# Kernel tuning notes

Measured on AMD Instinct MI355X. Metric: run time of the kernel, lower is better.

## Reference

```python
import jax, jax.numpy as jnp
import numpy as np

N = 50000
E = 625000
D = 128
L = 3
BN_EPS = 1e-5


def setup_inputs() -> dict:
    key = jax.random.key(0)
    ks = jax.random.split(key, 12)
    x = jax.random.normal(ks[0], (N, D), dtype=jnp.float32)
    edge_index = jax.random.randint(ks[1], (2, E), 0, N, dtype=jnp.int64)
    s = 1.0 / np.sqrt(D)
    W1 = jax.random.uniform(ks[2], (L, D, D), jnp.float32, -s, s)
    b1 = jax.random.uniform(ks[3], (L, D), jnp.float32, -s, s)
    W2 = jax.random.uniform(ks[4], (L, D, D), jnp.float32, -s, s)
    b2 = jax.random.uniform(ks[5], (L, D), jnp.float32, -s, s)
    eps = jnp.zeros((L,), jnp.float32)  # GINConv train_eps init 0
    gamma = jnp.ones((L, D), jnp.float32)
    beta = jnp.zeros((L, D), jnp.float32)
    Wl = jax.random.uniform(ks[6], (L, D, D), jnp.float32, -s, s)
    bl = jax.random.uniform(ks[7], (L, D), jnp.float32, -s, s)
    return {"x": x, "edge_index": edge_index, "W1": W1, "b1": b1, "W2": W2,
            "b2": b2, "eps": eps, "gamma": gamma, "beta": beta, "Wl": Wl, "bl": bl}


def reference(x, edge_index, W1, b1, W2, b2, eps, gamma, beta, Wl, bl):
    src, dst = edge_index[0], edge_index[1]
    xs = [x]
    h = x
    for i in range(L):
        # GIN aggregation: sum of neighbor (source) features at target nodes
        agg = jax.ops.segment_sum(h[src], dst, num_segments=N)  # [N, D]
        z = (1.0 + eps[i]) * h + agg
        # MLP: Linear -> ReLU -> Linear
        z = jax.nn.relu(z @ W1[i] + b1[i]) @ W2[i] + b2[i]
        # BatchNorm1d (training mode: batch stats, biased variance)
        mu = jnp.mean(z, axis=0)
        var = jnp.mean((z - mu) ** 2, axis=0)
        z = gamma[i] * (z - mu) * jax.lax.rsqrt(var + BN_EPS) + beta[i]
        if i != 0:
            z = z + xs[-1]
        h = jax.nn.relu(z)
        xs.append(h)
    outs = [xs[i + 1] @ Wl[i] + bl[i] for i in range(L)]
    return jnp.concatenate(outs, axis=-1)  # [N, L*D]
```

## Files before the change

### kernel.cpp

```cpp
#include <hip/hip_runtime.h>
#include <hip/hip_bf16.h>
#include <stdint.h>

#define NN 50000
#define NE 625000
#define DD 128
#define NL 3
#define GB 391

typedef __bf16 bf16x8 __attribute__((ext_vector_type(8)));
typedef float f32x4 __attribute__((ext_vector_type(4)));

__device__ __forceinline__ float bflo(uint32_t u) { return __uint_as_float(u << 16); }
__device__ __forceinline__ float bfhi(uint32_t u) { return __uint_as_float(u & 0xffff0000u); }
__device__ __forceinline__ uint16_t f2bf(float f) {
    __hip_bfloat16 h = __float2bfloat16(f);
    return __builtin_bit_cast(uint16_t, h);
}
__device__ __forceinline__ uint32_t pack2(float lo, float hi) {
    return (uint32_t)f2bf(lo) | ((uint32_t)f2bf(hi) << 16);
}

__global__ void k_hist(const int* __restrict__ dstv, int* __restrict__ deg) {
    int e = blockIdx.x * 256 + threadIdx.x;
    if (e < NE) atomicAdd(&deg[dstv[e]], 1);
}

__global__ __launch_bounds__(512) void k_scan1(int* __restrict__ cursor ,
                                               int* __restrict__ rowptr,
                                               int* __restrict__ rowend,
                                               int* __restrict__ gcount) {
    __shared__ int s[512];
    __shared__ int base;
    int t = threadIdx.x;
    int i = blockIdx.x * 512 + t;
    int v = (i < NN) ? cursor[i] : 0;
    s[t] = v;
    __syncthreads();
    for (int st = 1; st < 512; st <<= 1) {
        int a = (t >= st) ? s[t - st] : 0;
        __syncthreads();
        s[t] += a;
        __syncthreads();
    }
    if (t == 511) base = atomicAdd(gcount, s[511]);
    __syncthreads();
    if (i < NN) {
        int b = base + s[t] - v;
        rowptr[i] = b;
        rowend[i] = b + v;
        cursor[i] = b;
    }
}

__global__ void k_fill(const int* __restrict__ srcv, const int* __restrict__ dstv,
                       int* __restrict__ cursor, int* __restrict__ colv) {
    int e = blockIdx.x * 256 + threadIdx.x;
    if (e < NE) {
        int d = dstv[e];
        int p = atomicAdd(&cursor[d], 1);
        colv[p] = srcv[e];
    }
}

#define WCONV_BLOCKS 576
__global__ void k_prep(const float* __restrict__ x, uint16_t* __restrict__ hb,
                       int* __restrict__ cursor, int* __restrict__ gcount,
                       const float* __restrict__ W1, const float* __restrict__ W2,
                       const float* __restrict__ Wl, uint16_t* __restrict__ Wb) {
    int b = blockIdx.x;
    if (b < WCONV_BLOCKS) {
        int id = b * 256 + threadIdx.x;
        int m = id >> 14;
        int r = id & 16383;
        int k = r >> 7;
        int col = r & 127;
        const float* src;
        if (m < 3) src = W1 + m * 16384;
        else if (m < 6) src = W2 + (m - 3) * 16384;
        else src = Wl + (m - 6) * 16384;
        float v = src[k * 128 + col];
        Wb[m * 16384 + col * 128 + (k ^ ((col & 7) << 3))] = f2bf(v);
        return;
    }
    int id = (b - WCONV_BLOCKS) * 256 + threadIdx.x;
    if (id == 0) *gcount = 0;
    if (id < NN) cursor[id] = 0;
    int base = id * 4;
    if (base >= NN * DD) return;
    float4 v = *(const float4*)(x + base);
    uint2 st;
    st.x = pack2(v.x, v.y);
    st.y = pack2(v.z, v.w);
    *(uint2*)(hb + base) = st;
}

#define ACC8(u) \
    a0 += bflo(u.x); a1 += bfhi(u.x); a2 += bflo(u.y); a3 += bfhi(u.y); \
    a4 += bflo(u.z); a5 += bfhi(u.z); a6 += bflo(u.w); a7 += bfhi(u.w);

__global__ __launch_bounds__(256) void k_agg(const uint16_t* __restrict__ hb,
                                             const int* __restrict__ rowptr,
                                             const int* __restrict__ rowend,
                                             const int* __restrict__ colv,
                                             const float* __restrict__ epsp, int layer,
                                             uint16_t* __restrict__ zb,
                                             float* __restrict__ bnsum) {
    if (blockIdx.x == 0) bnsum[threadIdx.x] = 0.f;
    int g = (blockIdx.x * 256 + threadIdx.x) >> 4;
    int l16 = threadIdx.x & 15;
    if (g >= NN) return;
    float onepe = 1.0f + epsp[layer];
    int beg = rowptr[g], end = rowend[g];
    const uint4* hp = (const uint4*)hb;
    float a0 = 0.f, a1 = 0.f, a2 = 0.f, a3 = 0.f, a4 = 0.f, a5 = 0.f, a6 = 0.f, a7 = 0.f;
    int j = beg;
    for (; j + 7 < end; j += 8) {
        int s0 = colv[j];
        int s1 = colv[j + 1];
        int s2 = colv[j + 2];
        int s3 = colv[j + 3];
        int s4 = colv[j + 4];
        int s5 = colv[j + 5];
        int s6 = colv[j + 6];
        int s7 = colv[j + 7];
        uint4 u0 = hp[(size_t)s0 * 16 + l16];
        uint4 u1 = hp[(size_t)s1 * 16 + l16];
        uint4 u2 = hp[(size_t)s2 * 16 + l16];
        uint4 u3 = hp[(size_t)s3 * 16 + l16];
        uint4 u4 = hp[(size_t)s4 * 16 + l16];
        uint4 u5 = hp[(size_t)s5 * 16 + l16];
        uint4 u6 = hp[(size_t)s6 * 16 + l16];
        uint4 u7 = hp[(size_t)s7 * 16 + l16];
        ACC8(u0) ACC8(u1) ACC8(u2) ACC8(u3)
        ACC8(u4) ACC8(u5) ACC8(u6) ACC8(u7)
    }
    for (; j + 3 < end; j += 4) {
        int s0 = colv[j];
        int s1 = colv[j + 1];
        int s2 = colv[j + 2];
        int s3 = colv[j + 3];
        uint4 u0 = hp[(size_t)s0 * 16 + l16];
        uint4 u1 = hp[(size_t)s1 * 16 + l16];
        uint4 u2 = hp[(size_t)s2 * 16 + l16];
        uint4 u3 = hp[(size_t)s3 * 16 + l16];
        ACC8(u0) ACC8(u1) ACC8(u2) ACC8(u3)
    }
    for (; j < end; ++j) {
        int s0 = colv[j];
        uint4 u = hp[(size_t)s0 * 16 + l16];
        ACC8(u)
    }
    uint4 hu = hp[(size_t)g * 16 + l16];
    a0 = fmaf(onepe, bflo(hu.x), a0); a1 = fmaf(onepe, bfhi(hu.x), a1);
    a2 = fmaf(onepe, bflo(hu.y), a2); a3 = fmaf(onepe, bfhi(hu.y), a3);
    a4 = fmaf(onepe, bflo(hu.z), a4); a5 = fmaf(onepe, bfhi(hu.z), a5);
    a6 = fmaf(onepe, bflo(hu.w), a6); a7 = fmaf(onepe, bfhi(hu.w), a7);
    uint4 st;
    st.x = pack2(a0, a1); st.y = pack2(a2, a3);
    st.z = pack2(a4, a5); st.w = pack2(a6, a7);
    ((uint4*)zb)[(size_t)g * 16 + l16] = st;
}

__global__ __launch_bounds__(256) void k_mlp(const uint16_t* __restrict__ A,
                                             const uint16_t* __restrict__ W1img,
                                             const uint16_t* __restrict__ W2img,
                                             const float* __restrict__ b1,
                                             const float* __restrict__ b2,
                                             float* __restrict__ bnsum,
                                             uint16_t* __restrict__ z2b) {
    __shared__ uint16_t ldsW[16384];
    __shared__ uint16_t ldsT[16384];
    int tid = threadIdx.x;
    int wid = tid >> 6, lane = tid & 63;

    bf16x8 w2r[8];
#pragma unroll
    for (int it = 0; it < 8; ++it) w2r[it] = *(const bf16x8*)(W2img + (it * 256 + tid) * 8);

#pragma unroll
    for (int it = 0; it < 8; ++it) {
        int idx = (it * 256 + tid) * 8;
        *(bf16x8*)(&ldsW[idx]) = *(const bf16x8*)(W1img + idx);
    }
    __syncthreads();

    const int brow = blockIdx.x * 128;
    const int m0 = wid * 32;
    const int l15 = lane & 15;
    const int lhi = lane >> 4;

    f32x4 acc[2][8];
    f32x4 zero = {0.f, 0.f, 0.f, 0.f};
#pragma unroll
    for (int m = 0; m < 2; ++m)
#pragma unroll
        for (int n = 0; n < 8; ++n) acc[m][n] = zero;

    const char* Ab = (const char*)A;
#pragma unroll
    for (int kk = 0; kk < 4; ++kk) {
        int kbyte = kk * 64 + (lhi << 4);
        bf16x8 afrag[2];
#pragma unroll
        for (int m = 0; m < 2; ++m) {
            int row = brow + m0 + m * 16 + l15;
            if (row >= NN) row = NN - 1;
            afrag[m] = *(const bf16x8*)(Ab + (size_t)row * 256 + kbyte);
        }
#pragma unroll
        for (int n = 0; n < 8; ++n) {
            int col = n * 16 + l15;
            int addr = col * 256 + (kbyte ^ ((col & 7) << 4));
            bf16x8 bfrag = *(const bf16x8*)((const char*)ldsW + addr);
            acc[0][n] = __builtin_amdgcn_mfma_f32_16x16x32_bf16(afrag[0], bfrag, acc[0][n], 0, 0, 0);
            acc[1][n] = __builtin_amdgcn_mfma_f32_16x16x32_bf16(afrag[1], bfrag, acc[1][n], 0, 0, 0);
        }
    }

    {
        float bc[8];
#pragma unroll
        for (int n = 0; n < 8; ++n) bc[n] = b1[n * 16 + l15];
#pragma unroll
        for (int m = 0; m < 2; ++m) {
            int rbase = m0 + m * 16 + (lhi << 2);
#pragma unroll
            for (int r = 0; r < 4; ++r) {
                int row = rbase + r;
#pragma unroll
                for (int n = 0; n < 8; ++n) {
                    float v = fmaxf(acc[m][n][r] + bc[n], 0.f);
                    int col = n * 16 + l15;
                    int byteoff = row * 256 + ((col * 2) ^ ((row & 7) << 4));
                    *(uint16_t*)((char*)ldsT + byteoff) = f2bf(v);
                }
            }
        }
    }
    __syncthreads();

#pragma unroll
    for (int it = 0; it < 8; ++it) *(bf16x8*)(&ldsW[(it * 256 + tid) * 8]) = w2r[it];
    __syncthreads();

#pragma unroll
    for (int m = 0; m < 2; ++m)
#pragma unroll
        for (int n = 0; n < 8; ++n) acc[m][n] = zero;

#pragma unroll
    for (int kk = 0; kk < 4; ++kk) {
        int kbyte = kk * 64 + (lhi << 4);
        bf16x8 afrag[2];
#pragma unroll
        for (int m = 0; m < 2; ++m) {
            int rowl = m0 + m * 16 + l15;
            afrag[m] = *(const bf16x8*)((const char*)ldsT + rowl * 256 + (kbyte ^ ((rowl & 7) << 4)));
        }
#pragma unroll
        for (int n = 0; n < 8; ++n) {
            int col = n * 16 + l15;
            int addr = col * 256 + (kbyte ^ ((col & 7) << 4));
            bf16x8 bfrag = *(const bf16x8*)((const char*)ldsW + addr);
            acc[0][n] = __builtin_amdgcn_mfma_f32_16x16x32_bf16(afrag[0], bfrag, acc[0][n], 0, 0, 0);
            acc[1][n] = __builtin_amdgcn_mfma_f32_16x16x32_bf16(afrag[1], bfrag, acc[1][n], 0, 0, 0);
        }
    }

    float bc2[8];
#pragma unroll
    for (int n = 0; n < 8; ++n) bc2[n] = b2[n * 16 + l15];

    float s1[8], s2[8];
#pragma unroll
    for (int n = 0; n < 8; ++n) { s1[n] = 0.f; s2[n] = 0.f; }

#pragma unroll
    for (int m = 0; m < 2; ++m) {
        int rbase = brow + m0 + m * 16 + (lhi << 2);
#pragma unroll
        for (int r = 0; r < 4; ++r) {
            int row = rbase + r;
            bool ok = row < NN;
#pragma unroll
            for (int n = 0; n < 8; ++n) {
                float v = acc[m][n][r] + bc2[n];
                if (ok) {
                    z2b[(size_t)row * 128 + n * 16 + l15] = f2bf(v);
                    s1[n] += v;
                    s2[n] += v * v;
                }
            }
        }
    }

    __syncthreads();
    float* ls = (float*)ldsT;
    ls[tid] = 0.f;
    __syncthreads();
#pragma unroll
    for (int n = 0; n < 8; ++n) {
        float a1 = s1[n] + __shfl_xor(s1[n], 16);
        a1 += __shfl_xor(a1, 32);
        float a2 = s2[n] + __shfl_xor(s2[n], 16);
        a2 += __shfl_xor(a2, 32);
        if (lane < 16) {
            atomicAdd(&ls[n * 16 + lane], a1);
            atomicAdd(&ls[128 + n * 16 + lane], a2);
        }
    }
    __syncthreads();
    atomicAdd(&bnsum[tid], ls[tid]);
}

__global__ __launch_bounds__(256) void k_apply(const uint16_t* __restrict__ z2b,
                                               const uint16_t* __restrict__ hin,
                                               const float* __restrict__ bnsum,
                                               const float* __restrict__ gamma,
                                               const float* __restrict__ beta, int layer,
                                               uint16_t* __restrict__ hout) {
    __shared__ float sA[128], sB[128];
    int tid = threadIdx.x;
    if (tid < 128) {
        float mu = bnsum[tid] * (1.0f / NN);
        float var = bnsum[128 + tid] * (1.0f / NN) - mu * mu;
        float a = gamma[layer * 128 + tid] * rsqrtf(var + 1e-5f);
        sA[tid] = a;
        sB[tid] = beta[layer * 128 + tid] - mu * a;
    }
    __syncthreads();
    int id = blockIdx.x * 256 + tid;
    int base = id * 4;
    if (base >= NN * DD) return;
    int c = base & 127;
    uint2 zu = *(const uint2*)(z2b + base);
    float4 av = *(const float4*)(sA + c);
    float4 bv = *(const float4*)(sB + c);
    float v0 = fmaf(av.x, bflo(zu.x), bv.x);
    float v1 = fmaf(av.y, bfhi(zu.x), bv.y);
    float v2 = fmaf(av.z, bflo(zu.y), bv.z);
    float v3 = fmaf(av.w, bfhi(zu.y), bv.w);
    if (layer > 0) {
        uint2 h = *(const uint2*)(hin + base);
        v0 += bflo(h.x);
        v1 += bfhi(h.x);
        v2 += bflo(h.y);
        v3 += bfhi(h.y);
    }
    v0 = fmaxf(v0, 0.f);
    v1 = fmaxf(v1, 0.f);
    v2 = fmaxf(v2, 0.f);
    v3 = fmaxf(v3, 0.f);
    uint2 st;
    st.x = pack2(v0, v1);
    st.y = pack2(v2, v3);
    *(uint2*)(hout + base) = st;
}

__global__ __launch_bounds__(256) void k_outgemm(const uint16_t* __restrict__ h1,
                                                 const uint16_t* __restrict__ h2,
                                                 const uint16_t* __restrict__ h3,
                                                 const uint16_t* __restrict__ Wb6,
                                                 const float* __restrict__ bl,
                                                 float* __restrict__ out) {
    __shared__ uint16_t lds[16384];
    int layer = blockIdx.x / GB;
    int blk = blockIdx.x - layer * GB;
    const uint16_t* A = (layer == 0) ? h1 : ((layer == 1) ? h2 : h3);
    const uint16_t* Wimg = Wb6 + layer * 16384;
    const float* bias = bl + layer * 128;

    int tid = threadIdx.x;
    int wid = tid >> 6, lane = tid & 63;
#pragma unroll
    for (int it = 0; it < 8; ++it) {
        int idx = (it * 256 + tid) * 8;
        bf16x8 v = *(const bf16x8*)(Wimg + idx);
        *(bf16x8*)(&lds[idx]) = v;
    }
    __syncthreads();

    const int brow = blk * 128;
    const int m0 = wid * 32;
    const int l15 = lane & 15;
    const int lhi = lane >> 4;

    f32x4 acc[2][8];
    f32x4 zero = {0.f, 0.f, 0.f, 0.f};
#pragma unroll
    for (int m = 0; m < 2; ++m)
#pragma unroll
        for (int n = 0; n < 8; ++n) acc[m][n] = zero;

    const char* Ab = (const char*)A;
#pragma unroll
    for (int kk = 0; kk < 4; ++kk) {
        int kbyte = kk * 64 + (lhi << 4);
        bf16x8 afrag[2];
#pragma unroll
        for (int m = 0; m < 2; ++m) {
            int row = brow + m0 + m * 16 + l15;
            if (row >= NN) row = NN - 1;
            afrag[m] = *(const bf16x8*)(Ab + (size_t)row * 256 + kbyte);
        }
#pragma unroll
        for (int n = 0; n < 8; ++n) {
            int col = n * 16 + l15;
            int addr = col * 256 + (kbyte ^ ((col & 7) << 4));
            bf16x8 bfrag = *(const bf16x8*)((const char*)lds + addr);
            acc[0][n] = __builtin_amdgcn_mfma_f32_16x16x32_bf16(afrag[0], bfrag, acc[0][n], 0, 0, 0);
            acc[1][n] = __builtin_amdgcn_mfma_f32_16x16x32_bf16(afrag[1], bfrag, acc[1][n], 0, 0, 0);
        }
    }

    float bcol[8];
#pragma unroll
    for (int n = 0; n < 8; ++n) bcol[n] = bias[n * 16 + l15];

#pragma unroll
    for (int m = 0; m < 2; ++m) {
        int rbase = brow + m0 + m * 16 + (lhi << 2);
#pragma unroll
        for (int r = 0; r < 4; ++r) {
            int row = rbase + r;
            if (row < NN) {
#pragma unroll
                for (int n = 0; n < 8; ++n) {
                    float v = acc[m][n][r] + bcol[n];
                    out[(size_t)row * (NL * DD) + layer * 128 + n * 16 + l15] = v;
                }
            }
        }
    }
}

extern "C" void kernel_launch(void* const* d_in, const int* in_sizes, int n_in,
                              void* d_out, int out_size, void* d_ws, size_t ws_size,
                              hipStream_t stream) {
    const float* x = (const float*)d_in[0];
    const int* ei = (const int*)d_in[1];
    const float* W1 = (const float*)d_in[2];
    const float* b1 = (const float*)d_in[3];
    const float* W2 = (const float*)d_in[4];
    const float* b2 = (const float*)d_in[5];
    const float* epsp = (const float*)d_in[6];
    const float* gamma = (const float*)d_in[7];
    const float* beta = (const float*)d_in[8];
    const float* Wl = (const float*)d_in[9];
    const float* bl = (const float*)d_in[10];
    float* out = (float*)d_out;

    char* w = (char*)d_ws;
    size_t off = 0;
    auto take = [&](size_t b) -> char* {
        char* p = w + off;
        off += (b + 255) & ~(size_t)255;
        return p;
    };
    uint16_t* hb[4];
    for (int i = 0; i < 4; ++i) hb[i] = (uint16_t*)take((size_t)NN * DD * 2);
    uint16_t* zb = (uint16_t*)take((size_t)NN * DD * 2);
    uint16_t* z2b = (uint16_t*)take((size_t)NN * DD * 2);
    int* rowptr = (int*)take((size_t)NN * 4);
    int* rowend = (int*)take((size_t)NN * 4);
    int* cursor = (int*)take((size_t)NN * 4);
    int* colv = (int*)take((size_t)NE * 4);
    uint16_t* Wb = (uint16_t*)take(9 * 16384 * 2);
    float* bnsum = (float*)take(256 * 4);
    int* gcount = (int*)take(256);

    const int* srcv = ei;
    const int* dstv = ei + NE;

    const int x2bf_blocks = (NN * DD / 4 + 255) / 256;
    k_prep<<<WCONV_BLOCKS + x2bf_blocks, 256, 0, stream>>>(x, hb[0], cursor, gcount,
                                                           W1, W2, Wl, Wb);

    k_hist<<<(NE + 255) / 256, 256, 0, stream>>>(dstv, cursor);
    k_scan1<<<98, 512, 0, stream>>>(cursor, rowptr, rowend, gcount);
    k_fill<<<(NE + 255) / 256, 256, 0, stream>>>(srcv, dstv, cursor, colv);

    const int agg_blocks = (NN * 16 + 255) / 256;

    for (int l = 0; l < NL; ++l) {
        k_agg<<<agg_blocks, 256, 0, stream>>>(hb[l], rowptr, rowend, colv, epsp, l, zb, bnsum);
        k_mlp<<<GB, 256, 0, stream>>>(zb, Wb + l * 16384, Wb + (3 + l) * 16384,
                                      b1 + l * 128, b2 + l * 128, bnsum, z2b);
        k_apply<<<x2bf_blocks, 256, 0, stream>>>(z2b, hb[l], bnsum, gamma, beta,
                                                 l, hb[l + 1]);
    }
    k_outgemm<<<NL * GB, 256, 0, stream>>>(hb[1], hb[2], hb[3], Wb + 6 * 16384, bl, out);
}
```

Before: 266.2 us.

## Fuse aggregation into MLP kernel and BN-apply into output GEMM

```diff
diff --git a/kernel.cpp b/kernel.cpp
--- a/kernel.cpp
+++ b/kernel.cpp
@@ -66,6 +66,7 @@
 #define WCONV_BLOCKS 576
 __global__ void k_prep(const float* __restrict__ x, uint16_t* __restrict__ hb,
                        int* __restrict__ cursor, int* __restrict__ gcount,
+                       float* __restrict__ bnsum,
                        const float* __restrict__ W1, const float* __restrict__ W2,
                        const float* __restrict__ Wl, uint16_t* __restrict__ Wb) {
     int b = blockIdx.x;
@@ -85,6 +86,7 @@
     }
     int id = (b - WCONV_BLOCKS) * 256 + threadIdx.x;
     if (id == 0) *gcount = 0;
+    if (id < NL * 256) bnsum[id] = 0.f;
     if (id < NN) cursor[id] = 0;
     int base = id * 4;
     if (base >= NN * DD) return;
@@ -95,97 +97,110 @@
     *(uint2*)(hb + base) = st;
 }
 
-#define ACC8(u) \
-    a0 += bflo(u.x); a1 += bfhi(u.x); a2 += bflo(u.y); a3 += bfhi(u.y); \
-    a4 += bflo(u.z); a5 += bfhi(u.z); a6 += bflo(u.w); a7 += bfhi(u.w);
-
-__global__ __launch_bounds__(256) void k_agg(const uint16_t* __restrict__ hb,
-                                             const int* __restrict__ rowptr,
-                                             const int* __restrict__ rowend,
-                                             const int* __restrict__ colv,
-                                             const float* __restrict__ epsp, int layer,
-                                             uint16_t* __restrict__ zb,
-                                             float* __restrict__ bnsum) {
-    if (blockIdx.x == 0) bnsum[threadIdx.x] = 0.f;
-    int g = (blockIdx.x * 256 + threadIdx.x) >> 4;
-    int l16 = threadIdx.x & 15;
-    if (g >= NN) return;
-    float onepe = 1.0f + epsp[layer];
-    int beg = rowptr[g], end = rowend[g];
-    const uint4* hp = (const uint4*)hb;
-    float a0 = 0.f, a1 = 0.f, a2 = 0.f, a3 = 0.f, a4 = 0.f, a5 = 0.f, a6 = 0.f, a7 = 0.f;
-    int j = beg;
-    for (; j + 7 < end; j += 8) {
-        int s0 = colv[j];
-        int s1 = colv[j + 1];
-        int s2 = colv[j + 2];
-        int s3 = colv[j + 3];
-        int s4 = colv[j + 4];
-        int s5 = colv[j + 5];
-        int s6 = colv[j + 6];
-        int s7 = colv[j + 7];
-        uint4 u0 = hp[(size_t)s0 * 16 + l16];
-        uint4 u1 = hp[(size_t)s1 * 16 + l16];
-        uint4 u2 = hp[(size_t)s2 * 16 + l16];
-        uint4 u3 = hp[(size_t)s3 * 16 + l16];
-        uint4 u4 = hp[(size_t)s4 * 16 + l16];
-        uint4 u5 = hp[(size_t)s5 * 16 + l16];
-        uint4 u6 = hp[(size_t)s6 * 16 + l16];
-        uint4 u7 = hp[(size_t)s7 * 16 + l16];
-        ACC8(u0) ACC8(u1) ACC8(u2) ACC8(u3)
-        ACC8(u4) ACC8(u5) ACC8(u6) ACC8(u7)
-    }
-    for (; j + 3 < end; j += 4) {
-        int s0 = colv[j];
-        int s1 = colv[j + 1];
-        int s2 = colv[j + 2];
-        int s3 = colv[j + 3];
-        uint4 u0 = hp[(size_t)s0 * 16 + l16];
-        uint4 u1 = hp[(size_t)s1 * 16 + l16];
-        uint4 u2 = hp[(size_t)s2 * 16 + l16];
-        uint4 u3 = hp[(size_t)s3 * 16 + l16];
-        ACC8(u0) ACC8(u1) ACC8(u2) ACC8(u3)
-    }
-    for (; j < end; ++j) {
-        int s0 = colv[j];
-        uint4 u = hp[(size_t)s0 * 16 + l16];
-        ACC8(u)
-    }
-    uint4 hu = hp[(size_t)g * 16 + l16];
-    a0 = fmaf(onepe, bflo(hu.x), a0); a1 = fmaf(onepe, bfhi(hu.x), a1);
-    a2 = fmaf(onepe, bflo(hu.y), a2); a3 = fmaf(onepe, bfhi(hu.y), a3);
-    a4 = fmaf(onepe, bflo(hu.z), a4); a5 = fmaf(onepe, bfhi(hu.z), a5);
-    a6 = fmaf(onepe, bflo(hu.w), a6); a7 = fmaf(onepe, bfhi(hu.w), a7);
-    uint4 st;
-    st.x = pack2(a0, a1); st.y = pack2(a2, a3);
-    st.z = pack2(a4, a5); st.w = pack2(a6, a7);
-    ((uint4*)zb)[(size_t)g * 16 + l16] = st;
-}
-
-__global__ __launch_bounds__(256) void k_mlp(const uint16_t* __restrict__ A,
-                                             const uint16_t* __restrict__ W1img,
-                                             const uint16_t* __restrict__ W2img,
-                                             const float* __restrict__ b1,
-                                             const float* __restrict__ b2,
-                                             float* __restrict__ bnsum,
-                                             uint16_t* __restrict__ z2b) {
+__global__ __launch_bounds__(256) void k_aggmlp(const uint16_t* __restrict__ hb,
+                                                const int* __restrict__ rowptr,
+                                                const int* __restrict__ rowend,
+                                                const int* __restrict__ colv,
+                                                const float* __restrict__ epsp, int layer,
+                                                const uint16_t* __restrict__ W1img,
+                                                const uint16_t* __restrict__ W2img,
+                                                const float* __restrict__ b1,
+                                                const float* __restrict__ b2,
+                                                float* __restrict__ bnsum,
+                                                uint16_t* __restrict__ z2b) {
     __shared__ uint16_t ldsW[16384];
     __shared__ uint16_t ldsT[16384];
     int tid = threadIdx.x;
     int wid = tid >> 6, lane = tid & 63;
-
-    bf16x8 w2r[8];
-#pragma unroll
-    for (int it = 0; it < 8; ++it) w2r[it] = *(const bf16x8*)(W2img + (it * 256 + tid) * 8);
+    const int brow = blockIdx.x * 128;
 
 #pragma unroll
     for (int it = 0; it < 8; ++it) {
         int idx = (it * 256 + tid) * 8;
         *(bf16x8*)(&ldsW[idx]) = *(const bf16x8*)(W1img + idx);
     }
-    __syncthreads();
-
-    const int brow = blockIdx.x * 128;
+
+    int row = tid >> 1, half = tid & 1;
+    int g = brow + row;
+    float a[64];
+#pragma unroll
+    for (int i = 0; i < 64; ++i) a[i] = 0.f;
+    if (g < NN) {
+        float onepe = 1.0f + epsp[layer];
+        int beg = rowptr[g], end = rowend[g];
+        const uint4* hp = (const uint4*)hb + half * 8;
+        int j = beg;
+        for (; j + 1 < end; j += 2) {
+            int s0 = colv[j];
+            int s1 = colv[j + 1];
+            const uint4* r0 = hp + (size_t)s0 * 16;
+            const uint4* r1 = hp + (size_t)s1 * 16;
+            uint4 u[8], v[8];
+#pragma unroll
+            for (int i = 0; i < 8; ++i) u[i] = r0[i];
+#pragma unroll
+            for (int i = 0; i < 8; ++i) v[i] = r1[i];
+#pragma unroll
+            for (int i = 0; i < 8; ++i) {
+                a[i * 8 + 0] += bflo(u[i].x); a[i * 8 + 1] += bfhi(u[i].x);
+                a[i * 8 + 2] += bflo(u[i].y); a[i * 8 + 3] += bfhi(u[i].y);
+                a[i * 8 + 4] += bflo(u[i].z); a[i * 8 + 5] += bfhi(u[i].z);
+                a[i * 8 + 6] += bflo(u[i].w); a[i * 8 + 7] += bfhi(u[i].w);
+            }
+#pragma unroll
+            for (int i = 0; i < 8; ++i) {
+                a[i * 8 + 0] += bflo(v[i].x); a[i * 8 + 1] += bfhi(v[i].x);
+                a[i * 8 + 2] += bflo(v[i].y); a[i * 8 + 3] += bfhi(v[i].y);
+                a[i * 8 + 4] += bflo(v[i].z); a[i * 8 + 5] += bfhi(v[i].z);
+                a[i * 8 + 6] += bflo(v[i].w); a[i * 8 + 7] += bfhi(v[i].w);
+            }
+        }
+        if (j < end) {
+            int s0 = colv[j];
+            const uint4* r0 = hp + (size_t)s0 * 16;
+            uint4 u[8];
+#pragma unroll
+            for (int i = 0; i < 8; ++i) u[i] = r0[i];
+#pragma unroll
+            for (int i = 0; i < 8; ++i) {
+                a[i * 8 + 0] += bflo(u[i].x); a[i * 8 + 1] += bfhi(u[i].x);
+                a[i * 8 + 2] += bflo(u[i].y); a[i * 8 + 3] += bfhi(u[i].y);
+                a[i * 8 + 4] += bflo(u[i].z); a[i * 8 + 5] += bfhi(u[i].z);
+                a[i * 8 + 6] += bflo(u[i].w); a[i * 8 + 7] += bfhi(u[i].w);
+            }
+        }
+        {
+            const uint4* rs = hp + (size_t)g * 16;
+            uint4 u[8];
+#pragma unroll
+            for (int i = 0; i < 8; ++i) u[i] = rs[i];
+#pragma unroll
+            for (int i = 0; i < 8; ++i) {
+                a[i * 8 + 0] = fmaf(onepe, bflo(u[i].x), a[i * 8 + 0]);
+                a[i * 8 + 1] = fmaf(onepe, bfhi(u[i].x), a[i * 8 + 1]);
+                a[i * 8 + 2] = fmaf(onepe, bflo(u[i].y), a[i * 8 + 2]);
+                a[i * 8 + 3] = fmaf(onepe, bfhi(u[i].y), a[i * 8 + 3]);
+                a[i * 8 + 4] = fmaf(onepe, bflo(u[i].z), a[i * 8 + 4]);
+                a[i * 8 + 5] = fmaf(onepe, bfhi(u[i].z), a[i * 8 + 5]);
+                a[i * 8 + 6] = fmaf(onepe, bflo(u[i].w), a[i * 8 + 6]);
+                a[i * 8 + 7] = fmaf(onepe, bfhi(u[i].w), a[i * 8 + 7]);
+            }
+        }
+    }
+    {
+        int swz = (row & 7) << 4;
+#pragma unroll
+        for (int i = 0; i < 8; ++i) {
+            uint4 st;
+            st.x = pack2(a[i * 8 + 0], a[i * 8 + 1]);
+            st.y = pack2(a[i * 8 + 2], a[i * 8 + 3]);
+            st.z = pack2(a[i * 8 + 4], a[i * 8 + 5]);
+            st.w = pack2(a[i * 8 + 6], a[i * 8 + 7]);
+            *(uint4*)((char*)ldsT + row * 256 + ((half * 128 + i * 16) ^ swz)) = st;
+        }
+    }
+    __syncthreads();
+
     const int m0 = wid * 32;
     const int l15 = lane & 15;
     const int lhi = lane >> 4;
@@ -197,16 +212,14 @@
 #pragma unroll
         for (int n = 0; n < 8; ++n) acc[m][n] = zero;
 
-    const char* Ab = (const char*)A;
 #pragma unroll
     for (int kk = 0; kk < 4; ++kk) {
         int kbyte = kk * 64 + (lhi << 4);
         bf16x8 afrag[2];
 #pragma unroll
         for (int m = 0; m < 2; ++m) {
-            int row = brow + m0 + m * 16 + l15;
-            if (row >= NN) row = NN - 1;
-            afrag[m] = *(const bf16x8*)(Ab + (size_t)row * 256 + kbyte);
+            int rowl = m0 + m * 16 + l15;
+            afrag[m] = *(const bf16x8*)((const char*)ldsT + rowl * 256 + (kbyte ^ ((rowl & 7) << 4)));
         }
 #pragma unroll
         for (int n = 0; n < 8; ++n) {
@@ -227,12 +240,12 @@
             int rbase = m0 + m * 16 + (lhi << 2);
 #pragma unroll
             for (int r = 0; r < 4; ++r) {
-                int row = rbase + r;
+                int rw = rbase + r;
 #pragma unroll
                 for (int n = 0; n < 8; ++n) {
                     float v = fmaxf(acc[m][n][r] + bc[n], 0.f);
                     int col = n * 16 + l15;
-                    int byteoff = row * 256 + ((col * 2) ^ ((row & 7) << 4));
+                    int byteoff = rw * 256 + ((col * 2) ^ ((rw & 7) << 4));
                     *(uint16_t*)((char*)ldsT + byteoff) = f2bf(v);
                 }
             }
@@ -241,7 +254,10 @@
     __syncthreads();
 
 #pragma unroll
-    for (int it = 0; it < 8; ++it) *(bf16x8*)(&ldsW[(it * 256 + tid) * 8]) = w2r[it];
+    for (int it = 0; it < 8; ++it) {
+        int idx = (it * 256 + tid) * 8;
+        *(bf16x8*)(&ldsW[idx]) = *(const bf16x8*)(W2img + idx);
+    }
     __syncthreads();
 
 #pragma unroll
@@ -281,13 +297,13 @@
         int rbase = brow + m0 + m * 16 + (lhi << 2);
 #pragma unroll
         for (int r = 0; r < 4; ++r) {
-            int row = rbase + r;
-            bool ok = row < NN;
+            int rw = rbase + r;
+            bool ok = rw < NN;
 #pragma unroll
             for (int n = 0; n < 8; ++n) {
                 float v = acc[m][n][r] + bc2[n];
                 if (ok) {
-                    z2b[(size_t)row * 128 + n * 16 + l15] = f2bf(v);
+                    z2b[(size_t)rw * 128 + n * 16 + l15] = f2bf(v);
                     s1[n] += v;
                     s2[n] += v * v;
                 }
@@ -314,74 +330,88 @@
     atomicAdd(&bnsum[tid], ls[tid]);
 }
 
-__global__ __launch_bounds__(256) void k_apply(const uint16_t* __restrict__ z2b,
-                                               const uint16_t* __restrict__ hin,
-                                               const float* __restrict__ bnsum,
-                                               const float* __restrict__ gamma,
-                                               const float* __restrict__ beta, int layer,
-                                               uint16_t* __restrict__ hout) {
-    __shared__ float sA[128], sB[128];
-    int tid = threadIdx.x;
-    if (tid < 128) {
-        float mu = bnsum[tid] * (1.0f / NN);
-        float var = bnsum[128 + tid] * (1.0f / NN) - mu * mu;
-        float a = gamma[layer * 128 + tid] * rsqrtf(var + 1e-5f);
-        sA[tid] = a;
-        sB[tid] = beta[layer * 128 + tid] - mu * a;
-    }
-    __syncthreads();
-    int id = blockIdx.x * 256 + tid;
-    int base = id * 4;
-    if (base >= NN * DD) return;
-    int c = base & 127;
-    uint2 zu = *(const uint2*)(z2b + base);
-    float4 av = *(const float4*)(sA + c);
-    float4 bv = *(const float4*)(sB + c);
-    float v0 = fmaf(av.x, bflo(zu.x), bv.x);
-    float v1 = fmaf(av.y, bfhi(zu.x), bv.y);
-    float v2 = fmaf(av.z, bflo(zu.y), bv.z);
-    float v3 = fmaf(av.w, bfhi(zu.y), bv.w);
-    if (layer > 0) {
-        uint2 h = *(const uint2*)(hin + base);
-        v0 += bflo(h.x);
-        v1 += bfhi(h.x);
-        v2 += bflo(h.y);
-        v3 += bfhi(h.y);
-    }
-    v0 = fmaxf(v0, 0.f);
-    v1 = fmaxf(v1, 0.f);
-    v2 = fmaxf(v2, 0.f);
-    v3 = fmaxf(v3, 0.f);
-    uint2 st;
-    st.x = pack2(v0, v1);
-    st.y = pack2(v2, v3);
-    *(uint2*)(hout + base) = st;
-}
-
-__global__ __launch_bounds__(256) void k_outgemm(const uint16_t* __restrict__ h1,
-                                                 const uint16_t* __restrict__ h2,
-                                                 const uint16_t* __restrict__ h3,
-                                                 const uint16_t* __restrict__ Wb6,
-                                                 const float* __restrict__ bl,
-                                                 float* __restrict__ out) {
-    __shared__ uint16_t lds[16384];
-    int layer = blockIdx.x / GB;
-    int blk = blockIdx.x - layer * GB;
-    const uint16_t* A = (layer == 0) ? h1 : ((layer == 1) ? h2 : h3);
-    const uint16_t* Wimg = Wb6 + layer * 16384;
-    const float* bias = bl + layer * 128;
-
+__global__ __launch_bounds__(256) void k_applyout(const uint16_t* __restrict__ z2b,
+                                                  const uint16_t* __restrict__ hin,
+                                                  const float* __restrict__ bnsumL,
+                                                  const float* __restrict__ gammal,
+                                                  const float* __restrict__ betal,
+                                                  int has_skip,
+                                                  const uint16_t* __restrict__ Wlimg,
+                                                  const float* __restrict__ blv,
+                                                  uint16_t* __restrict__ hout,
+                                                  float* __restrict__ outl) {
+    __shared__ uint16_t ldsW[16384];
+    __shared__ uint16_t ldsT[16384];
+    __shared__ float sAB[256];
     int tid = threadIdx.x;
     int wid = tid >> 6, lane = tid & 63;
+    const int brow = blockIdx.x * 128;
+
 #pragma unroll
     for (int it = 0; it < 8; ++it) {
         int idx = (it * 256 + tid) * 8;
-        bf16x8 v = *(const bf16x8*)(Wimg + idx);
-        *(bf16x8*)(&lds[idx]) = v;
-    }
-    __syncthreads();
-
-    const int brow = blk * 128;
+        *(bf16x8*)(&ldsW[idx]) = *(const bf16x8*)(Wlimg + idx);
+    }
+    if (tid < 128) {
+        float mu = bnsumL[tid] * (1.0f / NN);
+        float var = bnsumL[128 + tid] * (1.0f / NN) - mu * mu;
+        float aa = gammal[tid] * rsqrtf(var + 1e-5f);
+        sAB[tid] = aa;
+        sAB[128 + tid] = betal[tid] - mu * aa;
+    }
+    __syncthreads();
+
+    int row = tid >> 1, half = tid & 1;
+    int g = brow + row;
+    {
+        int swz = (row & 7) << 4;
+        if (g < NN) {
+            const uint4* zrow = (const uint4*)(z2b + (size_t)g * 128) + half * 8;
+            const uint4* hrow = (const uint4*)(hin + (size_t)g * 128) + half * 8;
+            uint4* orow = (uint4*)(hout + (size_t)g * 128) + half * 8;
+            uint4 zu[8], hu[8];
+#pragma unroll
+            for (int i = 0; i < 8; ++i) zu[i] = zrow[i];
+            if (has_skip) {
+#pragma unroll
+                for (int i = 0; i < 8; ++i) hu[i] = hrow[i];
+            }
+#pragma unroll
+            for (int i = 0; i < 8; ++i) {
+                int c0 = half * 64 + i * 8;
+                float v[8];
+                v[0] = fmaf(sAB[c0 + 0], bflo(zu[i].x), sAB[128 + c0 + 0]);
+                v[1] = fmaf(sAB[c0 + 1], bfhi(zu[i].x), sAB[128 + c0 + 1]);
+                v[2] = fmaf(sAB[c0 + 2], bflo(zu[i].y), sAB[128 + c0 + 2]);
+                v[3] = fmaf(sAB[c0 + 3], bfhi(zu[i].y), sAB[128 + c0 + 3]);
+                v[4] = fmaf(sAB[c0 + 4], bflo(zu[i].z), sAB[128 + c0 + 4]);
+                v[5] = fmaf(sAB[c0 + 5], bfhi(zu[i].z), sAB[128 + c0 + 5]);
+                v[6] = fmaf(sAB[c0 + 6], bflo(zu[i].w), sAB[128 + c0 + 6]);
+                v[7] = fmaf(sAB[c0 + 7], bfhi(zu[i].w), sAB[128 + c0 + 7]);
+                if (has_skip) {
+                    v[0] += bflo(hu[i].x); v[1] += bfhi(hu[i].x);
+                    v[2] += bflo(hu[i].y); v[3] += bfhi(hu[i].y);
+                    v[4] += bflo(hu[i].z); v[5] += bfhi(hu[i].z);
+                    v[6] += bflo(hu[i].w); v[7] += bfhi(hu[i].w);
+                }
+#pragma unroll
+                for (int k = 0; k < 8; ++k) v[k] = fmaxf(v[k], 0.f);
+                uint4 st;
+                st.x = pack2(v[0], v[1]);
+                st.y = pack2(v[2], v[3]);
+                st.z = pack2(v[4], v[5]);
+                st.w = pack2(v[6], v[7]);
+                orow[i] = st;
+                *(uint4*)((char*)ldsT + row * 256 + ((half * 128 + i * 16) ^ swz)) = st;
+            }
+        } else {
+            uint4 zz = {0, 0, 0, 0};
+#pragma unroll
+            for (int i = 0; i < 8; ++i)
+                *(uint4*)((char*)ldsT + row * 256 + ((half * 128 + i * 16) ^ swz)) = zz;
+        }
+    }
+
     const int m0 = wid * 32;
     const int l15 = lane & 15;
     const int lhi = lane >> 4;
@@ -393,42 +423,39 @@
 #pragma unroll
         for (int n = 0; n < 8; ++n) acc[m][n] = zero;
 
-    const char* Ab = (const char*)A;
 #pragma unroll
     for (int kk = 0; kk < 4; ++kk) {
         int kbyte = kk * 64 + (lhi << 4);
         bf16x8 afrag[2];
 #pragma unroll
         for (int m = 0; m < 2; ++m) {
-            int row = brow + m0 + m * 16 + l15;
-            if (row >= NN) row = NN - 1;
-            afrag[m] = *(const bf16x8*)(Ab + (size_t)row * 256 + kbyte);
+            int rowl = m0 + m * 16 + l15;
+            afrag[m] = *(const bf16x8*)((const char*)ldsT + rowl * 256 + (kbyte ^ ((rowl & 7) << 4)));
         }
 #pragma unroll
         for (int n = 0; n < 8; ++n) {
             int col = n * 16 + l15;
             int addr = col * 256 + (kbyte ^ ((col & 7) << 4));
-            bf16x8 bfrag = *(const bf16x8*)((const char*)lds + addr);
+            bf16x8 bfrag = *(const bf16x8*)((const char*)ldsW + addr);
             acc[0][n] = __builtin_amdgcn_mfma_f32_16x16x32_bf16(afrag[0], bfrag, acc[0][n], 0, 0, 0);
             acc[1][n] = __builtin_amdgcn_mfma_f32_16x16x32_bf16(afrag[1], bfrag, acc[1][n], 0, 0, 0);
         }
     }
 
-    float bcol[8];
-#pragma unroll
-    for (int n = 0; n < 8; ++n) bcol[n] = bias[n * 16 + l15];
+    float bc3[8];
+#pragma unroll
+    for (int n = 0; n < 8; ++n) bc3[n] = blv[n * 16 + l15];
 
 #pragma unroll
     for (int m = 0; m < 2; ++m) {
         int rbase = brow + m0 + m * 16 + (lhi << 2);
 #pragma unroll
         for (int r = 0; r < 4; ++r) {
-            int row = rbase + r;
-            if (row < NN) {
+            int rw = rbase + r;
+            if (rw < NN) {
 #pragma unroll
                 for (int n = 0; n < 8; ++n) {
-                    float v = acc[m][n][r] + bcol[n];
-                    out[(size_t)row * (NL * DD) + layer * 128 + n * 16 + l15] = v;
+                    outl[(size_t)rw * (NL * DD) + n * 16 + l15] = acc[m][n][r] + bc3[n];
                 }
             }
         }
@@ -460,35 +487,35 @@
     };
     uint16_t* hb[4];
     for (int i = 0; i < 4; ++i) hb[i] = (uint16_t*)take((size_t)NN * DD * 2);
-    uint16_t* zb = (uint16_t*)take((size_t)NN * DD * 2);
     uint16_t* z2b = (uint16_t*)take((size_t)NN * DD * 2);
     int* rowptr = (int*)take((size_t)NN * 4);
     int* rowend = (int*)take((size_t)NN * 4);
     int* cursor = (int*)take((size_t)NN * 4);
     int* colv = (int*)take((size_t)NE * 4);
     uint16_t* Wb = (uint16_t*)take(9 * 16384 * 2);
-    float* bnsum = (float*)take(256 * 4);
+    float* bnsum = (float*)take(NL * 256 * 4);
     int* gcount = (int*)take(256);
 
     const int* srcv = ei;
     const int* dstv = ei + NE;
 
     const int x2bf_blocks = (NN * DD / 4 + 255) / 256;
-    k_prep<<<WCONV_BLOCKS + x2bf_blocks, 256, 0, stream>>>(x, hb[0], cursor, gcount,
+    k_prep<<<WCONV_BLOCKS + x2bf_blocks, 256, 0, stream>>>(x, hb[0], cursor, gcount, bnsum,
                                                            W1, W2, Wl, Wb);
 
     k_hist<<<(NE + 255) / 256, 256, 0, stream>>>(dstv, cursor);
     k_scan1<<<98, 512, 0, stream>>>(cursor, rowptr, rowend, gcount);
     k_fill<<<(NE + 255) / 256, 256, 0, stream>>>(srcv, dstv, cursor, colv);
 
-    const int agg_blocks = (NN * 16 + 255) / 256;
-
     for (int l = 0; l < NL; ++l) {
-        k_agg<<<agg_blocks, 256, 0, stream>>>(hb[l], rowptr, rowend, colv, epsp, l, zb, bnsum);
-        k_mlp<<<GB, 256, 0, stream>>>(zb, Wb + l * 16384, Wb + (3 + l) * 16384,
-                                      b1 + l * 128, b2 + l * 128, bnsum, z2b);
-        k_apply<<<x2bf_blocks, 256, 0, stream>>>(z2b, hb[l], bnsum, gamma, beta,
-                                                 l, hb[l + 1]);
-    }
-    k_outgemm<<<NL * GB, 256, 0, stream>>>(hb[1], hb[2], hb[3], Wb + 6 * 16384, bl, out);
-}
+        k_aggmlp<<<GB, 256, 0, stream>>>(hb[l], rowptr, rowend, colv, epsp, l,
+                                         Wb + l * 16384, Wb + (3 + l) * 16384,
+                                         b1 + l * 128, b2 + l * 128,
+                                         bnsum + l * 256, z2b);
+        k_applyout<<<GB, 256, 0, stream>>>(z2b, hb[l], bnsum + l * 256,
+                                           gamma + l * 128, beta + l * 128,
+                                           l > 0 ? 1 : 0,
+                                           Wb + (6 + l) * 16384, bl + l * 128,
+                                           hb[l + 1], out + l * 128);
+    }
+}
```

Result: slower. 322.0 us (+20.9%).
